# Kernel optimization log

Hardware: AMD Instinct MI355X
Metric: run time of the kernel (lower is better)

Reference implementation:

```python
import jax, jax.numpy as jnp
import numpy as np

N = 50000      # num_nodes
E = 800000     # num_edges (before self-loops)
IN_C = 128
HID = 64       # per-head channels (concat=False -> heads averaged)
HEADS = 4
OUT_C = 128
NEG_SLOPE = 0.2
EPS = 1e-5


def setup_inputs() -> dict:
    key = jax.random.key(0)
    ks = jax.random.split(key, 12)
    p = lambda k, shape: jax.random.normal(k, shape, dtype=jnp.float32) * 0.1
    inp = {
        "x": jax.random.normal(ks[0], (N, IN_C), dtype=jnp.float32),
        "edge_index": jax.random.randint(ks[1], (2, E), 0, N, dtype=jnp.int32),
        # layer 1 GATConv params
        "W1": p(ks[2], (IN_C, HEADS * HID)),
        "asrc1": p(ks[3], (HEADS, HID)),
        "adst1": p(ks[4], (HEADS, HID)),
        "b1": jnp.zeros((HID,), jnp.float32),
        "g1": jnp.ones((HID,), jnp.float32),
        "be1": jnp.zeros((HID,), jnp.float32),
        # layer 2 GATConv params
        "W2": p(ks[5], (HID, HEADS * HID)),
        "asrc2": p(ks[6], (HEADS, HID)),
        "adst2": p(ks[7], (HEADS, HID)),
        "b2": jnp.zeros((HID,), jnp.float32),
        "g2": jnp.ones((HID,), jnp.float32),
        "be2": jnp.zeros((HID,), jnp.float32),
        # output projection
        "Wo": p(ks[8], (HID, OUT_C)),
        "bo": jnp.zeros((OUT_C,), jnp.float32),
    }
    return inp


def _gat(x, W, asrc, adst, b, src, dst):
    """PyG GATConv (shared lin, concat=False -> mean over heads, + bias)."""
    n = x.shape[0]
    h = (x @ W).reshape(n, HEADS, HID)          # [N,H,C]
    es = jnp.sum(h * asrc, axis=-1)             # [N,H] alpha_src
    ed = jnp.sum(h * adst, axis=-1)             # [N,H] alpha_dst
    e = jax.nn.leaky_relu(es[src] + ed[dst], NEG_SLOPE)  # [E,H]
    # segment softmax over edges grouped by destination node
    emax = jax.ops.segment_max(e, dst, num_segments=n)
    ex = jnp.exp(e - emax[dst])
    den = jax.ops.segment_sum(ex, dst, num_segments=n)
    alpha = ex / den[dst]                       # [E,H]
    msg = h[src] * alpha[:, :, None]            # [E,H,C]
    out = jax.ops.segment_sum(msg, dst, num_segments=n)  # [N,H,C]
    return out.mean(axis=1) + b                 # concat=False -> head mean


def _ln(x, g, b):
    m = x.mean(-1, keepdims=True)
    v = x.var(-1, keepdims=True)
    return (x - m) / jnp.sqrt(v + EPS) * g + b


def reference(x, edge_index, W1, asrc1, adst1, b1, g1, be1,
              W2, asrc2, adst2, b2, g2, be2, Wo, bo):
    n = x.shape[0]
    loop = jnp.arange(n, dtype=edge_index.dtype)   # GATConv add_self_loops=True
    src = jnp.concatenate([edge_index[0], loop])
    dst = jnp.concatenate([edge_index[1], loop])
    h = jax.nn.relu(_ln(_gat(x, W1, asrc1, adst1, b1, src, dst), g1, be1))
    h = jax.nn.relu(_ln(_gat(h, W2, asrc2, adst2, b2, src, dst), g2, be2))
    return h @ Wo + bo
```

## Files before the change

kernel.cpp:

```cpp
#include <hip/hip_runtime.h>

#define NHEADS 4
#define NEG_SLOPE 0.2f
#define EPS_LN 1e-5f
#define BCAP 64

typedef __attribute__((ext_vector_type(8))) short bf16x8;
typedef __attribute__((ext_vector_type(4))) float f32x4;

__global__ __launch_bounds__(256) void k_init_deg(int* __restrict__ deg, int n) {
    int i = blockIdx.x * 256 + threadIdx.x;
    if (i < n) deg[i] = 1;
}

__global__ __launch_bounds__(256) void k_count(const int* __restrict__ dst, int* __restrict__ deg, int e) {
    int i = blockIdx.x * 256 + threadIdx.x;
    if (i < e) atomicAdd(&deg[dst[i]], 1);
}

__global__ __launch_bounds__(256) void k_scan1(const int* __restrict__ deg, int* __restrict__ rs,
                                               int* __restrict__ bsum, int n) {
    __shared__ int tmp[256];
    int tx = threadIdx.x;
    int i = blockIdx.x * 256 + tx;
    int v = (i < n) ? deg[i] : 0;
    tmp[tx] = v;
    __syncthreads();
    for (int off = 1; off < 256; off <<= 1) {
        int t = (tx >= off) ? tmp[tx - off] : 0;
        __syncthreads();
        tmp[tx] += t;
        __syncthreads();
    }
    if (i < n) rs[i] = tmp[tx] - v;
    if (tx == 255) bsum[blockIdx.x] = tmp[255];
}

__global__ __launch_bounds__(256) void k_scan2(int* __restrict__ bsum, int nb) {
    __shared__ int tmp[256];
    int tx = threadIdx.x;
    int v = (tx < nb) ? bsum[tx] : 0;
    tmp[tx] = v;
    __syncthreads();
    for (int off = 1; off < 256; off <<= 1) {
        int t = (tx >= off) ? tmp[tx - off] : 0;
        __syncthreads();
        tmp[tx] += t;
        __syncthreads();
    }
    if (tx < nb) bsum[tx] = tmp[tx] - v;
}

__global__ __launch_bounds__(256) void k_scan3(int* __restrict__ rs, int* __restrict__ cur,
                                               const int* __restrict__ bsum, int n, int total) {
    int i = blockIdx.x * 256 + threadIdx.x;
    if (i < n) {
        int r = rs[i] + bsum[blockIdx.x];
        rs[i] = r;
        cur[i] = r;
    }
    if (i == 0) rs[n] = total;
}

__global__ __launch_bounds__(256) void k_scatter(const int* __restrict__ src, const int* __restrict__ dst,
                                                 int* __restrict__ cur, int* __restrict__ col, int e, int n) {
    int i = blockIdx.x * 256 + threadIdx.x;
    if (i < e + n) {
        int s, d;
        if (i < e) { s = src[i]; d = dst[i]; }
        else       { s = i - e;  d = i - e;  }
        int p = atomicAdd(&cur[d], 1);
        col[p] = s;
    }
}

__device__ __forceinline__ unsigned short cvt_bf16(float x) {
    unsigned u = __float_as_uint(x);
    u += 0x7fffu + ((u >> 16) & 1u);
    return (unsigned short)(u >> 16);
}

__device__ __forceinline__ unsigned pack2_bf16(float a, float b) {
    return (unsigned)cvt_bf16(a) | ((unsigned)cvt_bf16(b) << 16);
}

__global__ __launch_bounds__(256) void k_gemm_gat(const float* __restrict__ A, const float* __restrict__ B,
                                                  const float* __restrict__ asrc, const float* __restrict__ adst,
                                                  unsigned short* __restrict__ Hb16, float* __restrict__ es,
                                                  float* __restrict__ ed, int M, int K,
                                                  const int* __restrict__ e_src, const int* __restrict__ e_dst,
                                                  int* __restrict__ cnt, int* __restrict__ buck,
                                                  int E, int do_scatter) {
    __shared__ unsigned short Al[128][136];
    __shared__ unsigned short Bt[128][136];
    int tid = threadIdx.x;
    int m0 = blockIdx.x * 128;
    int n0 = blockIdx.y * 128;
    if (do_scatter) {
        int gthreads = gridDim.x * gridDim.y * 256;
        int gid = (blockIdx.y * gridDim.x + blockIdx.x) * 256 + tid;
        int tot = E + M;
        for (int i = gid; i < tot; i += gthreads) {
            int s, d;
            if (i < E) { s = e_src[i]; d = e_dst[i]; }
            else       { s = i - E;    d = i - E;    }
            int p = atomicAdd(&cnt[d], 1);
            if (p < BCAP) buck[(size_t)d * BCAP + p] = s;
        }
    }
    {
        int n = (tid & 31) * 4;
        for (int k = tid >> 5; k < K; k += 8) {
            float4 b4 = *(const float4*)&B[(size_t)k * 256 + n0 + n];
            Bt[n + 0][k] = cvt_bf16(b4.x);
            Bt[n + 1][k] = cvt_bf16(b4.y);
            Bt[n + 2][k] = cvt_bf16(b4.z);
            Bt[n + 3][k] = cvt_bf16(b4.w);
        }
    }
    if (K == 128) {
#pragma unroll
        for (int it = 0; it < 16; it++) {
            int idx = it * 256 + tid;
            int row = idx >> 5;
            int kq = (idx & 31) << 2;
            float4 a4 = make_float4(0.f, 0.f, 0.f, 0.f);
            if (m0 + row < M) a4 = *(const float4*)&A[(size_t)(m0 + row) * 128 + kq];
            uint2 p;
            p.x = pack2_bf16(a4.x, a4.y);
            p.y = pack2_bf16(a4.z, a4.w);
            *(uint2*)&Al[row][kq] = p;
        }
    } else {
#pragma unroll
        for (int it = 0; it < 8; it++) {
            int idx = it * 256 + tid;
            int row = idx >> 4;
            int kq = (idx & 15) << 2;
            float4 a4 = make_float4(0.f, 0.f, 0.f, 0.f);
            if (m0 + row < M) a4 = *(const float4*)&A[(size_t)(m0 + row) * 64 + kq];
            uint2 p;
            p.x = pack2_bf16(a4.x, a4.y);
            p.y = pack2_bf16(a4.z, a4.w);
            *(uint2*)&Al[row][kq] = p;
        }
    }
    __syncthreads();
    int w = tid >> 6, lane = tid & 63;
    int quad = lane >> 4, col16 = lane & 15;
    int rw = (w >> 1) * 64;
    int ch = w & 1;
    int head = blockIdx.y * 2 + ch;
    f32x4 acc[4][4] = {};
    int kc = K >> 5;
    for (int c = 0; c < kc; c++) {
        int kb = c * 32 + quad * 8;
        bf16x8 afr[4], bfr[4];
#pragma unroll
        for (int i = 0; i < 4; i++)
            afr[i] = *(const bf16x8*)&Al[rw + i * 16 + col16][kb];
#pragma unroll
        for (int j = 0; j < 4; j++)
            bfr[j] = *(const bf16x8*)&Bt[ch * 64 + j * 16 + col16][kb];
#pragma unroll
        for (int i = 0; i < 4; i++)
#pragma unroll
            for (int j = 0; j < 4; j++)
                acc[i][j] = __builtin_amdgcn_mfma_f32_16x16x32_bf16(afr[i], bfr[j], acc[i][j], 0, 0, 0);
    }
    int mw = m0 + rw;
    float av[4], dv[4];
#pragma unroll
    for (int j = 0; j < 4; j++) {
        av[j] = asrc[head * 64 + j * 16 + col16];
        dv[j] = adst[head * 64 + j * 16 + col16];
    }
#pragma unroll
    for (int i = 0; i < 4; i++) {
#pragma unroll
        for (int r = 0; r < 4; r++) {
            int m = mw + i * 16 + quad * 4 + r;
            float se = acc[i][0][r] * av[0] + acc[i][1][r] * av[1]
                     + acc[i][2][r] * av[2] + acc[i][3][r] * av[3];
            float sd = acc[i][0][r] * dv[0] + acc[i][1][r] * dv[1]
                     + acc[i][2][r] * dv[2] + acc[i][3][r] * dv[3];
            se += __shfl_xor(se, 1, 64); sd += __shfl_xor(sd, 1, 64);
            se += __shfl_xor(se, 2, 64); sd += __shfl_xor(sd, 2, 64);
            se += __shfl_xor(se, 4, 64); sd += __shfl_xor(sd, 4, 64);
            se += __shfl_xor(se, 8, 64); sd += __shfl_xor(sd, 8, 64);
            if (m < M) {
#pragma unroll
                for (int j = 0; j < 4; j++)
                    Hb16[(size_t)m * 256 + head * 64 + j * 16 + col16] = cvt_bf16(acc[i][j][r]);
                if (col16 == 0) { es[m * 4 + head] = se; ed[m * 4 + head] = sd; }
            }
        }
    }
}

__global__ __launch_bounds__(256) void k_gemm(const float* __restrict__ A, const float* __restrict__ B,
                                              const float* __restrict__ bias, float* __restrict__ C,
                                              int M, int Nn, int K) {
    __shared__ unsigned short Al[128][72];
    __shared__ unsigned short Bt[128][72];
    int tid = threadIdx.x;
    int m0 = blockIdx.x * 128;
    {
        int n = (tid & 31) * 4;
        for (int k = tid >> 5; k < K; k += 8) {
            float4 b4 = *(const float4*)&B[(size_t)k * Nn + n];
            Bt[n + 0][k] = cvt_bf16(b4.x);
            Bt[n + 1][k] = cvt_bf16(b4.y);
            Bt[n + 2][k] = cvt_bf16(b4.z);
            Bt[n + 3][k] = cvt_bf16(b4.w);
        }
    }
#pragma unroll
    for (int it = 0; it < 8; it++) {
        int idx = it * 256 + tid;
        int row = idx >> 4;
        int kq = (idx & 15) << 2;
        float4 a4 = make_float4(0.f, 0.f, 0.f, 0.f);
        if (m0 + row < M) a4 = *(const float4*)&A[(size_t)(m0 + row) * 64 + kq];
        uint2 p;
        p.x = pack2_bf16(a4.x, a4.y);
        p.y = pack2_bf16(a4.z, a4.w);
        *(uint2*)&Al[row][kq] = p;
    }
    __syncthreads();
    int w = tid >> 6, lane = tid & 63;
    int quad = lane >> 4, col16 = lane & 15;
    int rw = (w >> 1) * 64;
    int ch = w & 1;
    f32x4 acc[4][4] = {};
    int kc = K >> 5;
    for (int c = 0; c < kc; c++) {
        int kb = c * 32 + quad * 8;
        bf16x8 afr[4], bfr[4];
#pragma unroll
        for (int i = 0; i < 4; i++)
            afr[i] = *(const bf16x8*)&Al[rw + i * 16 + col16][kb];
#pragma unroll
        for (int j = 0; j < 4; j++)
            bfr[j] = *(const bf16x8*)&Bt[ch * 64 + j * 16 + col16][kb];
#pragma unroll
        for (int i = 0; i < 4; i++)
#pragma unroll
            for (int j = 0; j < 4; j++)
                acc[i][j] = __builtin_amdgcn_mfma_f32_16x16x32_bf16(afr[i], bfr[j], acc[i][j], 0, 0, 0);
    }
    int mw = m0 + rw;
    float bv[4];
#pragma unroll
    for (int j = 0; j < 4; j++) bv[j] = bias[ch * 64 + j * 16 + col16];
#pragma unroll
    for (int i = 0; i < 4; i++) {
#pragma unroll
        for (int r = 0; r < 4; r++) {
            int m = mw + i * 16 + quad * 4 + r;
            if (m < M) {
#pragma unroll
                for (int j = 0; j < 4; j++)
                    C[(size_t)m * Nn + ch * 64 + j * 16 + col16] = acc[i][j][r] + bv[j];
            }
        }
    }
}

__global__ __launch_bounds__(256) void k_gat_aggregate(const unsigned* __restrict__ Hb, const float* __restrict__ es,
                                                       const float* __restrict__ ed, const int* __restrict__ rs,
                                                       const int* __restrict__ cnt, const int* __restrict__ col,
                                                       int bucketed, const float* __restrict__ b,
                                                       const float* __restrict__ g, const float* __restrict__ be,
                                                       float* __restrict__ out, int n) {
    int node = blockIdx.x * 4 + (threadIdx.x >> 6);
    int lane = threadIdx.x & 63;
    if (node >= n) return;
    int head = lane >> 4;
    int cp = lane & 15;
    float edv = ed[node * 4 + head];
    float acc0 = 0.f, acc1 = 0.f, acc2 = 0.f, acc3 = 0.f, den = 0.f;
    int i0, i1;
    if (bucketed) { i0 = node * BCAP; i1 = i0 + cnt[node]; }
    else          { i0 = rs[node];    i1 = rs[node + 1];   }
    int i = i0;
    for (; i + 3 < i1; i += 4) {
        int s0 = col[i], s1 = col[i + 1], s2 = col[i + 2], s3 = col[i + 3];
        float e0 = es[s0 * 4 + head];
        float e1 = es[s1 * 4 + head];
        float e2 = es[s2 * 4 + head];
        float e3 = es[s3 * 4 + head];
        uint2 u0 = *(const uint2*)&Hb[(size_t)s0 * 128 + lane * 2];
        uint2 u1 = *(const uint2*)&Hb[(size_t)s1 * 128 + lane * 2];
        uint2 u2 = *(const uint2*)&Hb[(size_t)s2 * 128 + lane * 2];
        uint2 u3 = *(const uint2*)&Hb[(size_t)s3 * 128 + lane * 2];
        e0 += edv; e1 += edv; e2 += edv; e3 += edv;
        e0 = fmaxf(e0, NEG_SLOPE * e0);
        e1 = fmaxf(e1, NEG_SLOPE * e1);
        e2 = fmaxf(e2, NEG_SLOPE * e2);
        e3 = fmaxf(e3, NEG_SLOPE * e3);
        float w0 = __expf(e0), w1 = __expf(e1), w2 = __expf(e2), w3 = __expf(e3);
        acc0 += w0 * __uint_as_float(u0.x << 16);
        acc1 += w0 * __uint_as_float(u0.x & 0xffff0000u);
        acc2 += w0 * __uint_as_float(u0.y << 16);
        acc3 += w0 * __uint_as_float(u0.y & 0xffff0000u);
        acc0 += w1 * __uint_as_float(u1.x << 16);
        acc1 += w1 * __uint_as_float(u1.x & 0xffff0000u);
        acc2 += w1 * __uint_as_float(u1.y << 16);
        acc3 += w1 * __uint_as_float(u1.y & 0xffff0000u);
        acc0 += w2 * __uint_as_float(u2.x << 16);
        acc1 += w2 * __uint_as_float(u2.x & 0xffff0000u);
        acc2 += w2 * __uint_as_float(u2.y << 16);
        acc3 += w2 * __uint_as_float(u2.y & 0xffff0000u);
        acc0 += w3 * __uint_as_float(u3.x << 16);
        acc1 += w3 * __uint_as_float(u3.x & 0xffff0000u);
        acc2 += w3 * __uint_as_float(u3.y << 16);
        acc3 += w3 * __uint_as_float(u3.y & 0xffff0000u);
        den += w0 + w1 + w2 + w3;
    }
    for (; i < i1; i++) {
        int s0 = col[i];
        float e0 = es[s0 * 4 + head] + edv;
        uint2 u0 = *(const uint2*)&Hb[(size_t)s0 * 128 + lane * 2];
        e0 = fmaxf(e0, NEG_SLOPE * e0);
        float w0 = __expf(e0);
        acc0 += w0 * __uint_as_float(u0.x << 16);
        acc1 += w0 * __uint_as_float(u0.x & 0xffff0000u);
        acc2 += w0 * __uint_as_float(u0.y << 16);
        acc3 += w0 * __uint_as_float(u0.y & 0xffff0000u);
        den += w0;
    }
    float rd = 1.f / den;
    float r0 = acc0 * rd, r1 = acc1 * rd, r2 = acc2 * rd, r3 = acc3 * rd;
    r0 += __shfl_xor(r0, 16, 64); r1 += __shfl_xor(r1, 16, 64);
    r2 += __shfl_xor(r2, 16, 64); r3 += __shfl_xor(r3, 16, 64);
    r0 += __shfl_xor(r0, 32, 64); r1 += __shfl_xor(r1, 32, 64);
    r2 += __shfl_xor(r2, 32, 64); r3 += __shfl_xor(r3, 32, 64);
    float4 bb = *(const float4*)&b[cp * 4];
    float v0 = 0.25f * r0 + bb.x;
    float v1 = 0.25f * r1 + bb.y;
    float v2 = 0.25f * r2 + bb.z;
    float v3 = 0.25f * r3 + bb.w;
    float s = v0 + v1 + v2 + v3;
    float q = v0 * v0 + v1 * v1 + v2 * v2 + v3 * v3;
    for (int off = 1; off < 16; off <<= 1) {
        s += __shfl_xor(s, off, 64);
        q += __shfl_xor(q, off, 64);
    }
    float mean = s * (1.f / 64.f);
    float var = q * (1.f / 64.f) - mean * mean;
    float rinv = rsqrtf(var + EPS_LN);
    float4 gg = *(const float4*)&g[cp * 4];
    float4 ee = *(const float4*)&be[cp * 4];
    if (head == 0) {
        float4 y;
        y.x = fmaxf((v0 - mean) * rinv * gg.x + ee.x, 0.f);
        y.y = fmaxf((v1 - mean) * rinv * gg.y + ee.y, 0.f);
        y.z = fmaxf((v2 - mean) * rinv * gg.z + ee.z, 0.f);
        y.w = fmaxf((v3 - mean) * rinv * gg.w + ee.w, 0.f);
        *(float4*)&out[(size_t)node * 64 + cp * 4] = y;
    }
}

extern "C" void kernel_launch(void* const* d_in, const int* in_sizes, int n_in,
                              void* d_out, int out_size, void* d_ws, size_t ws_size,
                              hipStream_t stream) {
    const float* x     = (const float*)d_in[0];
    const int*   eidx  = (const int*)d_in[1];
    const float* W1    = (const float*)d_in[2];
    const float* asrc1 = (const float*)d_in[3];
    const float* adst1 = (const float*)d_in[4];
    const float* b1    = (const float*)d_in[5];
    const float* g1    = (const float*)d_in[6];
    const float* be1   = (const float*)d_in[7];
    const float* W2    = (const float*)d_in[8];
    const float* asrc2 = (const float*)d_in[9];
    const float* adst2 = (const float*)d_in[10];
    const float* b2    = (const float*)d_in[11];
    const float* g2    = (const float*)d_in[12];
    const float* be2   = (const float*)d_in[13];
    const float* Wo    = (const float*)d_in[14];
    const float* bo    = (const float*)d_in[15];

    const int N = in_sizes[0] / 128;
    const int E = in_sizes[1] / 2;
    const int* srcp = eidx;
    const int* dstp = eidx + E;

    unsigned* hb   = (unsigned*)d_ws;
    float* h_small = (float*)(hb + (size_t)N * 128);
    float* es      = h_small + (size_t)N * 64;
    float* ed      = es + (size_t)N * 4;
    int* tail      = (int*)(ed + (size_t)N * 4);

    const int nb = (N + 255) / 256;
    const int nwb = (N + 3) / 4;
    const int mt128 = (N + 127) / 128;

    size_t prefix_bytes = (size_t)((char*)tail - (char*)d_ws);
    size_t bucket_need = prefix_bytes + (size_t)N * 4 + (size_t)N * BCAP * 4;

    int* rowstart = nullptr; int* colarr = nullptr; int* cnt = nullptr;
    bool bucketed = ws_size >= bucket_need;

    if (bucketed) {
        cnt    = tail;
        colarr = cnt + N;
        hipMemsetAsync(cnt, 0, (size_t)N * 4, stream);
    } else {
        int* deg  = tail;
        rowstart  = deg + N;
        int* cur  = rowstart + (N + 1);
        colarr    = cur + N;
        int* bsum = colarr + (size_t)(E + N);
        k_init_deg<<<nb, 256, 0, stream>>>(deg, N);
        k_count<<<(E + 255) / 256, 256, 0, stream>>>(dstp, deg, E);
        k_scan1<<<nb, 256, 0, stream>>>(deg, rowstart, bsum, N);
        k_scan2<<<1, 256, 0, stream>>>(bsum, nb);
        k_scan3<<<nb, 256, 0, stream>>>(rowstart, cur, bsum, N, E + N);
        k_scatter<<<(E + N + 255) / 256, 256, 0, stream>>>(srcp, dstp, cur, colarr, E, N);
    }
    int bflag = bucketed ? 1 : 0;

    k_gemm_gat<<<dim3(mt128, 2), 256, 0, stream>>>(x, W1, asrc1, adst1,
                                                   (unsigned short*)hb, es, ed, N, 128,
                                                   srcp, dstp, cnt, colarr, E, bflag);
    k_gat_aggregate<<<nwb, 256, 0, stream>>>(hb, es, ed, rowstart, cnt, colarr, bflag,
                                             b1, g1, be1, h_small, N);

    k_gemm_gat<<<dim3(mt128, 2), 256, 0, stream>>>(h_small, W2, asrc2, adst2,
                                                   (unsigned short*)hb, es, ed, N, 64,
                                                   srcp, dstp, cnt, colarr, E, 0);
    k_gat_aggregate<<<nwb, 256, 0, stream>>>(hb, es, ed, rowstart, cnt, colarr, bflag,
                                             b2, g2, be2, h_small, N);

    k_gemm<<<mt128, 256, 0, stream>>>(h_small, Wo, bo, (float*)d_out, N, 128, 64);
}
```

Before: 350.2 us.

## Load A fragments directly from global memory and vectorize B transpose stores

The GAT projection GEMM no longer stages the A tile in shared memory. Each wave reads its A rows straight from global memory as float4 pairs and converts them to bf16 fragments in registers. The B-to-Bt transpose in both GEMM kernels now has each thread handle one column and a k-range, writing packed 4-element bf16 stores instead of scalar 2-byte LDS writes. This halves LDS usage and removes bank-conflicting scattered stores. In exchange, A rows are reread from global or L2 by both column-half waves, and the per-lane loads are less coalesced.

```diff
diff --git a/kernel.cpp b/kernel.cpp
--- a/kernel.cpp
+++ b/kernel.cpp
@@ -91,7 +91,6 @@
                                                   const int* __restrict__ e_src, const int* __restrict__ e_dst,
                                                   int* __restrict__ cnt, int* __restrict__ buck,
                                                   int E, int do_scatter) {
-    __shared__ unsigned short Al[128][136];
     __shared__ unsigned short Bt[128][136];
     int tid = threadIdx.x;
     int m0 = blockIdx.x * 128;
@@ -109,46 +108,26 @@
         }
     }
     {
-        int n = (tid & 31) * 4;
-        for (int k = tid >> 5; k < K; k += 8) {
-            float4 b4 = *(const float4*)&B[(size_t)k * 256 + n0 + n];
-            Bt[n + 0][k] = cvt_bf16(b4.x);
-            Bt[n + 1][k] = cvt_bf16(b4.y);
-            Bt[n + 2][k] = cvt_bf16(b4.z);
-            Bt[n + 3][k] = cvt_bf16(b4.w);
-        }
-    }
-    if (K == 128) {
-#pragma unroll
-        for (int it = 0; it < 16; it++) {
-            int idx = it * 256 + tid;
-            int row = idx >> 5;
-            int kq = (idx & 31) << 2;
-            float4 a4 = make_float4(0.f, 0.f, 0.f, 0.f);
-            if (m0 + row < M) a4 = *(const float4*)&A[(size_t)(m0 + row) * 128 + kq];
+        int n = tid & 127;
+        int kh = tid >> 7;
+        int kbeg = kh * (K >> 1);
+        int kend = kbeg + (K >> 1);
+        const float* bp = B + n0 + n;
+        for (int k = kbeg; k < kend; k += 4) {
+            float b0 = bp[(size_t)k * 256];
+            float b1 = bp[(size_t)(k + 1) * 256];
+            float b2 = bp[(size_t)(k + 2) * 256];
+            float b3 = bp[(size_t)(k + 3) * 256];
             uint2 p;
-            p.x = pack2_bf16(a4.x, a4.y);
-            p.y = pack2_bf16(a4.z, a4.w);
-            *(uint2*)&Al[row][kq] = p;
-        }
-    } else {
-#pragma unroll
-        for (int it = 0; it < 8; it++) {
-            int idx = it * 256 + tid;
-            int row = idx >> 4;
-            int kq = (idx & 15) << 2;
-            float4 a4 = make_float4(0.f, 0.f, 0.f, 0.f);
-            if (m0 + row < M) a4 = *(const float4*)&A[(size_t)(m0 + row) * 64 + kq];
-            uint2 p;
-            p.x = pack2_bf16(a4.x, a4.y);
-            p.y = pack2_bf16(a4.z, a4.w);
-            *(uint2*)&Al[row][kq] = p;
+            p.x = pack2_bf16(b0, b1);
+            p.y = pack2_bf16(b2, b3);
+            *(uint2*)&Bt[n][k] = p;
         }
     }
     __syncthreads();
     int w = tid >> 6, lane = tid & 63;
     int quad = lane >> 4, col16 = lane & 15;
-    int rw = (w >> 1) * 64;
+    int mw = m0 + (w >> 1) * 64;
     int ch = w & 1;
     int head = blockIdx.y * 2 + ch;
     f32x4 acc[4][4] = {};
@@ -157,8 +136,19 @@
         int kb = c * 32 + quad * 8;
         bf16x8 afr[4], bfr[4];
 #pragma unroll
-        for (int i = 0; i < 4; i++)
-            afr[i] = *(const bf16x8*)&Al[rw + i * 16 + col16][kb];
+        for (int i = 0; i < 4; i++) {
+            int row = mw + i * 16 + col16;
+            if (row >= M) row = M - 1;
+            const float* ap = &A[(size_t)row * K + kb];
+            float4 a0 = *(const float4*)ap;
+            float4 a1 = *(const float4*)(ap + 4);
+            bf16x8 t;
+            t[0] = (short)cvt_bf16(a0.x); t[1] = (short)cvt_bf16(a0.y);
+            t[2] = (short)cvt_bf16(a0.z); t[3] = (short)cvt_bf16(a0.w);
+            t[4] = (short)cvt_bf16(a1.x); t[5] = (short)cvt_bf16(a1.y);
+            t[6] = (short)cvt_bf16(a1.z); t[7] = (short)cvt_bf16(a1.w);
+            afr[i] = t;
+        }
 #pragma unroll
         for (int j = 0; j < 4; j++)
             bfr[j] = *(const bf16x8*)&Bt[ch * 64 + j * 16 + col16][kb];
@@ -168,7 +158,6 @@
             for (int j = 0; j < 4; j++)
                 acc[i][j] = __builtin_amdgcn_mfma_f32_16x16x32_bf16(afr[i], bfr[j], acc[i][j], 0, 0, 0);
     }
-    int mw = m0 + rw;
     float av[4], dv[4];
 #pragma unroll
     for (int j = 0; j < 4; j++) {
@@ -206,13 +195,20 @@
     int tid = threadIdx.x;
     int m0 = blockIdx.x * 128;
     {
-        int n = (tid & 31) * 4;
-        for (int k = tid >> 5; k < K; k += 8) {
-            float4 b4 = *(const float4*)&B[(size_t)k * Nn + n];
-            Bt[n + 0][k] = cvt_bf16(b4.x);
-            Bt[n + 1][k] = cvt_bf16(b4.y);
-            Bt[n + 2][k] = cvt_bf16(b4.z);
-            Bt[n + 3][k] = cvt_bf16(b4.w);
+        int n = tid & 127;
+        int kh = tid >> 7;
+        int kbeg = kh * (K >> 1);
+        int kend = kbeg + (K >> 1);
+        const float* bp = B + n;
+        for (int k = kbeg; k < kend; k += 4) {
+            float b0 = bp[(size_t)k * Nn];
+            float b1 = bp[(size_t)(k + 1) * Nn];
+            float b2 = bp[(size_t)(k + 2) * Nn];
+            float b3 = bp[(size_t)(k + 3) * Nn];
+            uint2 p;
+            p.x = pack2_bf16(b0, b1);
+            p.y = pack2_bf16(b2, b3);
+            *(uint2*)&Bt[n][k] = p;
         }
     }
 #pragma unroll
```

After: 339.7 us. -3.0%, faster.
